# Kernel optimization log

Measured on AMD Instinct MI355X. Metric: run time of the kernel, lower is better.

Reference implementation:

```python
import jax, jax.numpy as jnp
import numpy as np
from jax import lax

DN = ('NCHW', 'OIHW', 'NCHW')


def conv3x3(x, w, b):
    y = lax.conv_general_dilated(x, w, (1, 1), [(1, 1), (1, 1)], dimension_numbers=DN)
    return y + b[None, :, None, None]


def lrelu(x, s):
    return jnp.where(x >= 0, x, s * x)


def layernorm_c(x, g, b, eps=1e-5):
    # LayerNorm over embed_dim; tokens are (h,w), so normalize the channel axis
    m = jnp.mean(x, axis=1, keepdims=True)
    v = jnp.var(x, axis=1, keepdims=True)
    return (x - m) / jnp.sqrt(v + eps) * g[None, :, None, None] + b[None, :, None, None]


def bilateral_corr(x1, x2, md):
    # bilateral cost volume on L2-normalized features:
    # out[b,d,h,w] = <x1n[b,:,h-dy,w-dx], x2n[b,:,h+dy,w+dx]>, (dy,dx) in [-md,md]^2
    def l2n(x):
        return x / jnp.maximum(jnp.linalg.norm(x, axis=1, keepdims=True), 1e-12)
    x1n, x2n = l2n(x1), l2n(x2)
    B, C, H, W = x1.shape
    p1 = jnp.pad(x1n, ((0, 0), (0, 0), (md, md), (md, md)))
    p2 = jnp.pad(x2n, ((0, 0), (0, 0), (md, md), (md, md)))
    outs = []
    for dy in range(-md, md + 1):
        for dx in range(-md, md + 1):
            a = p1[:, :, md - dy:md - dy + H, md - dx:md - dx + W]
            b = p2[:, :, md + dy:md + dy + H, md + dx:md + dx + W]
            outs.append(jnp.sum(a * b, axis=1))
    return jnp.stack(outs, axis=1)  # [B, (2md+1)^2, H, W]


def tail(xt, bi, gln, bln, w0, b0, wr1, br1, wr2, br2, w2, b2, w3, b3, wdec, bdec, wf, bf):
    xt = layernorm_c(xt, gln, bln)
    y = conv3x3(jnp.concatenate([xt, bi], axis=1), w0, b0)
    # resblock(64,64): lrelu(conv2(lrelu(conv1(y))) + y), slope 0.1
    s = y
    r = lrelu(conv3x3(y, wr1, br1), 0.1)
    r = conv3x3(r, wr2, br2) + s
    y = lrelu(r, 0.1)
    y = lrelu(conv3x3(y, w2, b2), 0.2)
    y = lrelu(conv3x3(y, w3, b3), 0.2)
    # ConvTranspose2d(64,64,3,stride=2,pad=1,out_pad=1): lhs-dilated conv with flipped kernel
    wd = jnp.transpose(jnp.flip(wdec, (-2, -1)), (1, 0, 2, 3))  # torch [in,out,kh,kw] -> OIHW
    y = lax.conv_general_dilated(y, wd, (1, 1), [(1, 2), (1, 2)], lhs_dilation=(2, 2), dimension_numbers=DN) + bdec[None, :, None, None]
    flow = conv3x3(y, wf, bf)  # [B, 2, 2H, 2W]
    B, _, H2, W2 = flow.shape
    # F.interpolate(scale_factor=4, mode='bilinear', align_corners=False) * 4
    return jax.image.resize(flow, (B, 2, 4 * H2, 4 * W2), method='bilinear') * 4.0


def setup_inputs():
    key = jax.random.key(0)
    ks = jax.random.split(key, 16)
    B, C, H, W = 4, 256, 96, 160
    md = 3
    r = lambda k, s, sc=0.05: jax.random.normal(k, s, jnp.float32) * sc
    return {
        'x1': jax.random.normal(ks[0], (B, C, H, W), jnp.float32),
        'x2': jax.random.normal(ks[1], (B, C, H, W), jnp.float32),
        'xt': jax.random.normal(ks[2], (B, C, H, W), jnp.float32),
        'gln': jnp.ones((C,), jnp.float32),
        'bln': jnp.zeros((C,), jnp.float32),
        'w0': r(ks[3], (64, C + (2 * md + 1) ** 2, 3, 3)),
        'b0': jnp.zeros((64,), jnp.float32),
        'wr1': r(ks[4], (64, 64, 3, 3)), 'br1': jnp.zeros((64,), jnp.float32),
        'wr2': r(ks[5], (64, 64, 3, 3)), 'br2': jnp.zeros((64,), jnp.float32),
        'w2': r(ks[6], (64, 64, 3, 3)), 'b2': jnp.zeros((64,), jnp.float32),
        'w3': r(ks[7], (64, 64, 3, 3)), 'b3': jnp.zeros((64,), jnp.float32),
        'wdec': r(ks[8], (64, 64, 3, 3)), 'bdec': jnp.zeros((64,), jnp.float32),
        'wf': r(ks[9], (2, 64, 3, 3)), 'bf': jnp.zeros((2,), jnp.float32),
        'corr_range': 3,
    }


def reference(x1, x2, xt, gln, bln, w0, b0, wr1, br1, wr2, br2, w2, b2, w3, b3, wdec, bdec, wf, bf, corr_range):
    bi = bilateral_corr(x1, x2, int(corr_range))
    return tail(xt, bi, gln, bln, w0, b0, wr1, br1, wr2, br2, w2, b2, w3, b3, wdec, bdec, wf, bf)
```

## Files before the change

### kernel.cpp

```cpp
#include <hip/hip_runtime.h>
#include <math.h>

#define HH_ 96
#define WW_ 160
#define HW 15360
#define NPIX 61440
#define CC 256
#define C0 320
#define FF 64
#define H2 192
#define W2 320
#define OHW 61440
#define HO 768
#define WO 1280

typedef __attribute__((ext_vector_type(8))) short short8;
typedef __attribute__((ext_vector_type(4))) float f32x4;

__device__ __forceinline__ float bf2f(ushort u) {
    union { unsigned int i; float f; } v; v.i = ((unsigned int)u) << 16; return v.f;
}
__device__ __forceinline__ ushort f2bf(float f) {
    union { float f; unsigned int i; } v; v.f = f;
    unsigned int u = v.i;
    return (ushort)((u + 0x7FFFu + ((u >> 16) & 1u)) >> 16);
}

__global__ __launch_bounds__(256) void normpack_kernel(
    const float* __restrict__ x1, const float* __restrict__ x2, const float* __restrict__ xt,
    const float* __restrict__ gam, const float* __restrict__ bet,
    ushort* __restrict__ x1c, ushort* __restrict__ x2c,
    ushort* __restrict__ Xhi, float* __restrict__ inv1, float* __restrict__ inv2) {
    __shared__ ushort tile[64 * 258];
    __shared__ float sred[4][64][2];
    const int t = threadIdx.x;
    const int w = t >> 6, l = t & 63;
    const int px4 = l & 15, c_off = l >> 4;
    const int pxt = blockIdx.x, which = blockIdx.y, b = blockIdx.z;
    const float* src = (which == 0 ? x1 : which == 1 ? x2 : xt);
    src += (size_t)b * CC * HW + pxt * 64;

    float s1[4] = {0.f, 0.f, 0.f, 0.f}, s2[4] = {0.f, 0.f, 0.f, 0.f};
#pragma unroll
    for (int it = 0; it < 16; ++it) {
        int c = it * 16 + w * 4 + c_off;
        f32x4 v4 = *(const f32x4*)(src + (size_t)c * HW + px4 * 4);
#pragma unroll
        for (int j = 0; j < 4; ++j) {
            float f = v4[j];
            s1[j] += f; s2[j] += f * f;
            tile[(px4 * 4 + j) * 258 + c] = f2bf(f);
        }
    }
#pragma unroll
    for (int j = 0; j < 4; ++j) {
        s1[j] += __shfl_xor(s1[j], 16); s1[j] += __shfl_xor(s1[j], 32);
        s2[j] += __shfl_xor(s2[j], 16); s2[j] += __shfl_xor(s2[j], 32);
    }
    if (c_off == 0) {
#pragma unroll
        for (int j = 0; j < 4; ++j) {
            sred[w][px4 * 4 + j][0] = s1[j];
            sred[w][px4 * 4 + j][1] = s2[j];
        }
    }
    __syncthreads();

    const int px = t >> 2, grp = t & 3;
    float S1 = sred[0][px][0] + sred[1][px][0] + sred[2][px][0] + sred[3][px][0];
    float S2 = sred[0][px][1] + sred[1][px][1] + sred[2][px][1] + sred[3][px][1];
    const int p = b * HW + pxt * 64 + px;
    const ushort* row = &tile[px * 258];
    if (which < 2) {
        float inv = 1.f / fmaxf(sqrtf(S2), 1e-12f);
        if (grp == 0) (which == 0 ? inv1 : inv2)[p] = inv;
        ushort* dst = (which == 0 ? x1c : x2c) + (size_t)p * CC + grp * 64;
#pragma unroll
        for (int k = 0; k < 8; ++k) {
            short8 o;
#pragma unroll
            for (int h = 0; h < 4; ++h) {
                unsigned int u2 = *(const unsigned int*)(row + grp * 64 + k * 8 + h * 2);
                o[h * 2]     = (short)(u2 & 0xFFFF);
                o[h * 2 + 1] = (short)(u2 >> 16);
            }
            *(short8*)(dst + k * 8) = o;
        }
    } else {
        float m = S1 * (1.f / 256.f);
        float var = fmaxf(S2 * (1.f / 256.f) - m * m, 0.f);
        float rs = rsqrtf(var + 1e-5f);
        ushort* dst = Xhi + (size_t)p * C0 + grp * 64;
#pragma unroll
        for (int k = 0; k < 8; ++k) {
            short8 o;
#pragma unroll
            for (int h = 0; h < 4; ++h) {
                unsigned int u2 = *(const unsigned int*)(row + grp * 64 + k * 8 + h * 2);
                int c = grp * 64 + k * 8 + h * 2;
                float f0 = (bf2f((ushort)(u2 & 0xFFFF)) - m) * rs * gam[c] + bet[c];
                float f1 = (bf2f((ushort)(u2 >> 16)) - m) * rs * gam[c + 1] + bet[c + 1];
                o[h * 2]     = (short)f2bf(f0);
                o[h * 2 + 1] = (short)f2bf(f1);
            }
            *(short8*)(dst + k * 8) = o;
        }
        short8 z = {0, 0, 0, 0, 0, 0, 0, 0};
        *(short8*)(Xhi + (size_t)p * C0 + 256 + grp * 16) = z;
        *(short8*)(Xhi + (size_t)p * C0 + 256 + grp * 16 + 8) = z;
    }
}

__global__ __launch_bounds__(256) void corr_mfma_kernel(
    const ushort* __restrict__ x1c, const ushort* __restrict__ x2c,
    const float* __restrict__ inv1, const float* __restrict__ inv2,
    ushort* __restrict__ Xhi) {
    const int lane = threadIdx.x & 63;
    const int wv = threadIdx.x >> 6;
    const int sid = ((blockIdx.x & 7) * 120) + (blockIdx.x >> 3);
    const int b  = sid / 240;
    const int rem = sid % 240;
    const int uq = rem / 10, xt = rem % 10;
    const int u = uq * 4 + wv;
    const int x0 = xt * 16;
    const int jl = lane & 15;
    const int kg = lane >> 4;
    const short8 zero8 = {0, 0, 0, 0, 0, 0, 0, 0};

    short8 qf[8];
    {
        size_t qb = ((size_t)b * HW + u * WW_ + x0 + jl) * CC + kg * 8;
#pragma unroll
        for (int ks = 0; ks < 8; ++ks)
            qf[ks] = *(const short8*)(x1c + qb + ks * 32);
    }
    float iv1v[4];
#pragma unroll
    for (int r = 0; r < 4; ++r)
        iv1v[r] = inv1[b * HW + u * WW_ + x0 + kg * 4 + r];

    for (int dy = -3; dy <= 3; ++dy) {
        const int y = u + dy;
        if ((unsigned)y >= (unsigned)HH_) continue;
        const int w = u + 2 * dy;
        const bool rowok = (unsigned)w < (unsigned)HH_;

        f32x4 acc0 = (f32x4){0.f, 0.f, 0.f, 0.f};
        f32x4 acc1 = (f32x4){0.f, 0.f, 0.f, 0.f};
        if (rowok) {
#pragma unroll
            for (int nt = 0; nt < 2; ++nt) {
                int kx = x0 - 6 + jl + 16 * nt;
                bool ok = (unsigned)kx < (unsigned)WW_;
                int kxc = min(max(kx, 0), WW_ - 1);
                size_t kb = ((size_t)b * HW + w * WW_ + kxc) * CC + kg * 8;
#pragma unroll
                for (int ks = 0; ks < 8; ++ks) {
                    short8 bv = *(const short8*)(x2c + kb + ks * 32);
                    if (!ok) bv = zero8;
                    if (nt == 0)
                        acc0 = __builtin_amdgcn_mfma_f32_16x16x32_bf16(qf[ks], bv, acc0, 0, 0, 0);
                    else
                        acc1 = __builtin_amdgcn_mfma_f32_16x16x32_bf16(qf[ks], bv, acc1, 0, 0, 0);
                }
            }
        }
#pragma unroll
        for (int nt = 0; nt < 2; ++nt) {
            int j = jl + 16 * nt;
#pragma unroll
            for (int r = 0; r < 4; ++r) {
                int q = kg * 4 + r;
                int tt = j - q - 6;
                if (tt & 1) continue;
                int dx = tt >> 1;
                if (dx < -3 || dx > 3) continue;
                int cx = x0 + q + dx;
                if ((unsigned)cx >= (unsigned)WW_) continue;
                float v = 0.f;
                if (rowok) {
                    int pbx = min(max(x0 + q + 2 * dx, 0), WW_ - 1);
                    float iv2 = inv2[b * HW + w * WW_ + pbx];
                    v = (nt == 0 ? acc0[r] : acc1[r]) * iv1v[r] * iv2;
                }
                size_t o = ((size_t)(b * HW + y * WW_ + cx)) * C0
                         + 256 + (dy + 3) * 7 + (dx + 3);
                Xhi[o] = f2bf(v);
            }
        }
    }
}

__global__ void pack_w_all(const float* __restrict__ w0, const float* __restrict__ wr1,
                           const float* __restrict__ wr2, const float* __restrict__ w2,
                           const float* __restrict__ w3, const float* __restrict__ wdec,
                           ushort* __restrict__ W0, ushort* __restrict__ WR1,
                           ushort* __restrict__ WR2, ushort* __restrict__ W2o,
                           ushort* __restrict__ W3o, ushort* __restrict__ WD) {
    int job = blockIdx.y;
    const float* w = job == 0 ? w0 : job == 1 ? wr1 : job == 2 ? wr2
                   : job == 3 ? w2 : job == 4 ? w3 : wdec;
    ushort* dst = job == 0 ? W0 : job == 1 ? WR1 : job == 2 ? WR2
                : job == 3 ? W2o : job == 4 ? W3o : WD;
    int CinReal = job == 0 ? 305 : 64;
    int KC = job == 0 ? 10 : 2;
    int isDeconv = (job == 5);
    int gid = blockIdx.x * blockDim.x + threadIdx.x;
    int total = 9 * KC * 4 * 64;
    if (gid >= total) return;
    int lane = gid & 63;
    int nt = (gid >> 6) & 3;
    int kc = (gid >> 8) % KC;
    int slot = (gid >> 8) / KC;
    int co = nt * 16 + (lane & 15);
    int ky = slot / 3, kx = slot % 3;
    for (int j = 0; j < 8; ++j) {
        int ci = kc * 32 + (lane >> 4) * 8 + j;
        float v = 0.f;
        if (ci < CinReal) {
            if (isDeconv) v = w[((size_t)(ci * 64 + co) * 3 + (2 - ky)) * 3 + (2 - kx)];
            else          v = w[((size_t)(co * CinReal + ci) * 3 + ky) * 3 + kx];
        }
        dst[(size_t)gid * 8 + j] = f2bf(v);
    }
}

template<int KC>
__global__ __launch_bounds__(256, 4) void conv_lds_t(
    const ushort* __restrict__ Ahi,
    const ushort* __restrict__ Whi,
    const float* __restrict__ bias,
    ushort* __restrict__ Ohi,
    const ushort* __restrict__ Rhi,
    float slope, int act, int hasres) {
    constexpr int CIN = KC * 32;
    __shared__ ushort lds[2 * 3488];
    const int t = threadIdx.x;
    const int lane = t & 63;
    const int wave = t >> 6;
    const int kg = lane >> 4;
    const int jl = lane & 15;
    const short8 zero8 = {0, 0, 0, 0, 0, 0, 0, 0};

    const int sid = ((blockIdx.x & 7) * 120) + (blockIdx.x >> 3);
    const int b0 = sid / 240;
    const int rm = sid % 240;
    const int yq = rm / 10, xw = rm % 10;
    const int y0 = yq * 4;
    const int x0 = xw * 16;
    const size_t rowbase = (size_t)b0 * HW;

    f32x4 acc[4];
#pragma unroll
    for (int nt = 0; nt < 4; ++nt) acc[nt] = (f32x4){0.f, 0.f, 0.f, 0.f};

    auto stage = [&](ushort* buf, int kc) {
#pragma unroll
        for (int i = 0; i < 2; ++i) {
            int e = t + i * 256;
            if (e < 432) {
                int kge = e & 3;
                int q = e >> 2;
                int pe = q % 18;
                int re = q / 18;
                int gy = y0 - 1 + re, gx = x0 - 1 + pe;
                bool ok = ((unsigned)gy < 96u) && ((unsigned)gx < 160u);
                short8 vh = zero8;
                if (ok) {
                    size_t ga = ((rowbase + gy * WW_ + gx) * (size_t)CIN) + kc * 32 + kge * 8;
                    vh = *(const short8*)(Ahi + ga);
                }
                *(short8*)(buf + kge * 872 + (re * 18 + pe) * 8) = vh;
            }
        }
    };

    stage(lds, 0);

#pragma unroll 1
    for (int kc = 0; kc < KC; ++kc) {
        __syncthreads();
        if (kc + 1 < KC) stage(lds + ((kc + 1) & 1) * 3488, kc + 1);
        const ushort* bufc = lds + (kc & 1) * 3488;
#pragma unroll
        for (int tap = 0; tap < 9; ++tap) {
            const int dy = tap / 3 - 1, dx = tap % 3 - 1;
            const int abase = kg * 872 + (wave + dy + 1) * 144 + (jl + dx + 1) * 8;
            short8 ah = *(const short8*)(bufc + abase);
            const ushort* wt = Whi + (size_t)(tap * KC + kc) * 2048;
#pragma unroll
            for (int nt = 0; nt < 4; ++nt) {
                short8 bh = *(const short8*)(wt + (nt * 64 + lane) * 8);
                acc[nt] = __builtin_amdgcn_mfma_f32_16x16x32_bf16(ah, bh, acc[nt], 0, 0, 0);
            }
        }
    }

#pragma unroll
    for (int r = 0; r < 4; ++r) {
        size_t pr = rowbase + (y0 + wave) * WW_ + x0 + kg * 4 + r;
#pragma unroll
        for (int nt = 0; nt < 4; ++nt) {
            int co = nt * 16 + jl;
            float vv = acc[nt][r] + bias[co];
            size_t oo = pr * 64 + co;
            if (hasres) vv += bf2f(Rhi[oo]);
            if (act) vv = vv >= 0.f ? vv : vv * slope;
            Ohi[oo] = f2bf(vv);
        }
    }
}

__global__ __launch_bounds__(256, 2) void deconv_fused_kernel(
    const ushort* __restrict__ Ahi,
    const ushort* __restrict__ Whi,
    const float* __restrict__ bias,
    ushort* __restrict__ decb) {
    const int lane = threadIdx.x & 63;
    const int wave = threadIdx.x >> 6;
    const int kg = lane >> 4;
    const short8 zero8 = {0, 0, 0, 0, 0, 0, 0, 0};

    const int sid = ((blockIdx.x & 7) * 120) + (blockIdx.x >> 3);
    const int b0 = sid / 240;
    const int rm = sid % 240;
    const int yq = rm / 10, xh = rm % 10;
    const int y0 = yq * 4 + wave;
    const int x0 = xh * 16;
    const size_t rowbase = (size_t)b0 * HW;

    f32x4 acc[4][4];
#pragma unroll
    for (int p = 0; p < 4; ++p)
#pragma unroll
        for (int nt = 0; nt < 4; ++nt) acc[p][nt] = (f32x4){0.f, 0.f, 0.f, 0.f};

    const int nuse[4]   = {4, 2, 2, 1};
    const int upar[4][4] = {{0, 1, 2, 3}, {1, 3, -1, -1}, {2, 3, -1, -1}, {3, -1, -1, -1}};
    const int uslt[4][4] = {{4, 3, 1, 0}, {5, 2, -1, -1}, {7, 6, -1, -1}, {8, -1, -1, -1}};

#pragma unroll
    for (int o = 0; o < 4; ++o) {
        const int ody = o >> 1, odx = o & 1;
        int yy = y0 + ody, xx = x0 + (lane & 15) + odx;
        bool v = (unsigned)yy < 96u && (unsigned)xx < 160u;
        int yyc = min(yy, 95), xxc = min(xx, 159);
        size_t a = (rowbase + yyc * WW_ + xxc) * 64 + kg * 8;
#pragma unroll
        for (int kc = 0; kc < 2; ++kc) {
            short8 ah = *(const short8*)(Ahi + a + kc * 32);
            if (!v) ah = zero8;
#pragma unroll
            for (int u = 0; u < 4; ++u) {
                if (u >= nuse[o]) break;
                int par = upar[o][u], slot = uslt[o][u];
#pragma unroll
                for (int nt = 0; nt < 4; ++nt) {
                    short8 bh = *(const short8*)(Whi + ((size_t)slot * 2 + kc) * 2048
                                                 + ((size_t)nt * 64 + lane) * 8);
                    acc[par][nt] = __builtin_amdgcn_mfma_f32_16x16x32_bf16(ah, bh, acc[par][nt], 0, 0, 0);
                }
            }
        }
    }

#pragma unroll
    for (int r = 0; r < 4; ++r) {
        int x2 = x0 + kg * 4 + r;
#pragma unroll
        for (int par = 0; par < 4; ++par) {
            int py = par >> 1, px = par & 1;
            size_t po = ((size_t)b0 * H2 + 2 * y0 + py) * W2 + 2 * x2 + px;
#pragma unroll
            for (int nt = 0; nt < 4; ++nt) {
                int co = nt * 16 + (lane & 15);
                decb[po * 64 + co] = f2bf(acc[par][nt][r] + bias[co]);
            }
        }
    }
}

__global__ __launch_bounds__(256) void flow_kernel(const ushort* __restrict__ decb,
                                                   const float* __restrict__ wf,
                                                   const float* __restrict__ bf2v,
                                                   float* __restrict__ flow) {
    __shared__ float wsm[1152];
    for (int i = threadIdx.x; i < 1152; i += 256) wsm[i] = wf[i];
    __syncthreads();
    int fid = ((blockIdx.x & 7) * 120) + (blockIdx.x >> 3);
    int p = fid * 256 + threadIdx.x;
    if (p >= 4 * OHW) return;
    int b = p / OHW, rem = p % OHW, oy = rem / W2, ox = rem % W2;
    float a0 = bf2v[0], a1 = bf2v[1];
    for (int ky = 0; ky < 3; ++ky) {
        int yy = oy + ky - 1;
        if ((unsigned)yy >= (unsigned)H2) continue;
        for (int kx = 0; kx < 3; ++kx) {
            int xx = ox + kx - 1;
            if ((unsigned)xx >= (unsigned)W2) continue;
            size_t base = ((size_t)b * OHW + yy * W2 + xx) * 64;
            int tap = ky * 3 + kx;
#pragma unroll
            for (int c8 = 0; c8 < 8; ++c8) {
                short8 v8 = *(const short8*)(decb + base + c8 * 8);
#pragma unroll
                for (int j = 0; j < 8; ++j) {
                    float f = bf2f((ushort)v8[j]);
                    int ci = c8 * 8 + j;
                    a0 += f * wsm[ci * 9 + tap];
                    a1 += f * wsm[(64 + ci) * 9 + tap];
                }
            }
        }
    }
    flow[(size_t)(b * 2 + 0) * OHW + rem] = a0;
    flow[(size_t)(b * 2 + 1) * OHW + rem] = a1;
}

__global__ __launch_bounds__(256) void resize_kernel(const float* __restrict__ flow,
                                                     float* __restrict__ out) {
    int idx = blockIdx.x * blockDim.x + threadIdx.x;
    int total = 4 * 2 * HO * (WO / 4);
    if (idx >= total) return;
    int qx = idx % (WO / 4);
    int oy = (idx / (WO / 4)) % HO;
    int c  = (idx / ((WO / 4) * HO)) % 2;
    int b  = idx / ((WO / 4) * HO * 2);

    float sy = (oy + 0.5f) * 0.25f - 0.5f;
    int y0 = (int)floorf(sy);
    float fy = sy - y0;
    int y0c = min(max(y0, 0), H2 - 1);
    int y1c = min(max(y0 + 1, 0), H2 - 1);
    const float* r0 = flow + ((size_t)(b * 2 + c) * H2 + y0c) * W2;
    const float* r1 = flow + ((size_t)(b * 2 + c) * H2 + y1c) * W2;
    int xm = max(qx - 1, 0), xp = min(qx + 1, W2 - 1);
    float fm = (1.f - fy) * r0[xm] + fy * r1[xm];
    float f0 = (1.f - fy) * r0[qx] + fy * r1[qx];
    float fp = (1.f - fy) * r0[xp] + fy * r1[xp];
    f32x4 o;
    o[0] = (0.375f * fm + 0.625f * f0) * 4.0f;
    o[1] = (0.125f * fm + 0.875f * f0) * 4.0f;
    o[2] = (0.875f * f0 + 0.125f * fp) * 4.0f;
    o[3] = (0.625f * f0 + 0.375f * fp) * 4.0f;
    *(f32x4*)(out + (((size_t)(b * 2 + c) * HO + oy) * WO) + qx * 4) = o;
}

extern "C" void kernel_launch(void* const* d_in, const int* in_sizes, int n_in,
                              void* d_out, int out_size, void* d_ws, size_t ws_size,
                              hipStream_t stream) {
    const float* x1   = (const float*)d_in[0];
    const float* x2   = (const float*)d_in[1];
    const float* xt   = (const float*)d_in[2];
    const float* gln  = (const float*)d_in[3];
    const float* bln  = (const float*)d_in[4];
    const float* w0   = (const float*)d_in[5];
    const float* b0   = (const float*)d_in[6];
    const float* wr1  = (const float*)d_in[7];
    const float* br1  = (const float*)d_in[8];
    const float* wr2  = (const float*)d_in[9];
    const float* br2  = (const float*)d_in[10];
    const float* w2   = (const float*)d_in[11];
    const float* b2   = (const float*)d_in[12];
    const float* w3   = (const float*)d_in[13];
    const float* b3   = (const float*)d_in[14];
    const float* wdec = (const float*)d_in[15];
    const float* bdec = (const float*)d_in[16];
    const float* wf   = (const float*)d_in[17];
    const float* bfv  = (const float*)d_in[18];
    float* out = (float*)d_out;

    char* ws = (char*)d_ws;
    ushort* x1c  = (ushort*)(ws + 0);
    ushort* x2c  = (ushort*)(ws + 31457280);
    ushort* X0hi = (ushort*)(ws + 62914560);
    ushort* y0hi = (ushort*)(ws + 102236160);
    ushort* t1hi = (ushort*)(ws + 110100480);
    ushort* t2hi = (ushort*)(ws + 117964800);
    ushort* decb = (ushort*)(ws + 0);
    float*  flowb = (float*)(ws + 62914560);
    char* wp = ws + 125829120;
    ushort* W0hi  = (ushort*)(wp);
    ushort* WR1hi = (ushort*)(wp + 368640);
    ushort* WR2hi = (ushort*)(wp + 442368);
    ushort* W2hi  = (ushort*)(wp + 516096);
    ushort* W3hi  = (ushort*)(wp + 589824);
    ushort* WDhi  = (ushort*)(wp + 663552);
    float*  inv1  = (float*)(wp + 786432);
    float*  inv2  = (float*)(wp + 1048576);

    pack_w_all<<<dim3(90, 6), 256, 0, stream>>>(w0, wr1, wr2, w2, w3, wdec,
        W0hi, WR1hi, WR2hi, W2hi, W3hi, WDhi);

    normpack_kernel<<<dim3(240, 3, 4), 256, 0, stream>>>(
        x1, x2, xt, gln, bln, x1c, x2c, X0hi, inv1, inv2);
    corr_mfma_kernel<<<960, 256, 0, stream>>>(x1c, x2c, inv1, inv2, X0hi);

    conv_lds_t<10><<<960, 256, 0, stream>>>(X0hi, W0hi, b0, y0hi, nullptr, 0.f, 0, 0);
    conv_lds_t<2><<<960, 256, 0, stream>>>(y0hi, WR1hi, br1, t1hi, nullptr, 0.1f, 1, 0);
    conv_lds_t<2><<<960, 256, 0, stream>>>(t1hi, WR2hi, br2, t2hi, y0hi, 0.1f, 1, 1);
    conv_lds_t<2><<<960, 256, 0, stream>>>(t2hi, W2hi, b2, t1hi, nullptr, 0.2f, 1, 0);
    conv_lds_t<2><<<960, 256, 0, stream>>>(t1hi, W3hi, b3, t2hi, nullptr, 0.2f, 1, 0);
    deconv_fused_kernel<<<960, 256, 0, stream>>>(t2hi, WDhi, bdec, decb);

    flow_kernel<<<960, 256, 0, stream>>>(decb, wf, bfv, flowb);
    resize_kernel<<<7680, 256, 0, stream>>>(flowb, out);

    (void)in_sizes; (void)n_in; (void)out_size; (void)ws_size;
}
```

Measured before the change: 357.7 us.

## Split work across more blocks in normpack, 64-ch convs, deconv and flow

Halves the per-block tile in normpack (32 pixels) and gives the 64-channel convs a new kernel where each block covers 2 rows and each wave computes only half of the output channels, with the LDS halo double-buffered over the two K chunks. The deconv also splits output channels across wave pairs, and the flow kernel splits the 64 input channels across two threads that combine their sums with a shuffle. Grids double to 1920 blocks and launch bounds are raised to allow more resident blocks per CU. The aim is better occupancy and latency hiding on small grids, at the cost of more redundant halo loads, and each wave now reuses its loaded activations across fewer MFMAs.

```diff
diff --git a/kernel.cpp b/kernel.cpp
--- a/kernel.cpp
+++ b/kernel.cpp
@@ -31,19 +31,20 @@
     const float* __restrict__ gam, const float* __restrict__ bet,
     ushort* __restrict__ x1c, ushort* __restrict__ x2c,
     ushort* __restrict__ Xhi, float* __restrict__ inv1, float* __restrict__ inv2) {
-    __shared__ ushort tile[64 * 258];
-    __shared__ float sred[4][64][2];
+    __shared__ ushort tile[32 * 258];
+    __shared__ float sred[4][32][2];
     const int t = threadIdx.x;
     const int w = t >> 6, l = t & 63;
-    const int px4 = l & 15, c_off = l >> 4;
+    const int px4 = l & 7;
+    const int cbase = t >> 3;
     const int pxt = blockIdx.x, which = blockIdx.y, b = blockIdx.z;
     const float* src = (which == 0 ? x1 : which == 1 ? x2 : xt);
-    src += (size_t)b * CC * HW + pxt * 64;
+    src += (size_t)b * CC * HW + pxt * 32;
 
     float s1[4] = {0.f, 0.f, 0.f, 0.f}, s2[4] = {0.f, 0.f, 0.f, 0.f};
 #pragma unroll
-    for (int it = 0; it < 16; ++it) {
-        int c = it * 16 + w * 4 + c_off;
+    for (int it = 0; it < 8; ++it) {
+        int c = it * 32 + cbase;
         f32x4 v4 = *(const f32x4*)(src + (size_t)c * HW + px4 * 4);
 #pragma unroll
         for (int j = 0; j < 4; ++j) {
@@ -54,10 +55,10 @@
     }
 #pragma unroll
     for (int j = 0; j < 4; ++j) {
-        s1[j] += __shfl_xor(s1[j], 16); s1[j] += __shfl_xor(s1[j], 32);
-        s2[j] += __shfl_xor(s2[j], 16); s2[j] += __shfl_xor(s2[j], 32);
-    }
-    if (c_off == 0) {
+        s1[j] += __shfl_xor(s1[j], 8);  s1[j] += __shfl_xor(s1[j], 16); s1[j] += __shfl_xor(s1[j], 32);
+        s2[j] += __shfl_xor(s2[j], 8);  s2[j] += __shfl_xor(s2[j], 16); s2[j] += __shfl_xor(s2[j], 32);
+    }
+    if ((l >> 3) == 0) {
 #pragma unroll
         for (int j = 0; j < 4; ++j) {
             sred[w][px4 * 4 + j][0] = s1[j];
@@ -66,21 +67,21 @@
     }
     __syncthreads();
 
-    const int px = t >> 2, grp = t & 3;
+    const int px = t >> 3, grp = t & 7;
     float S1 = sred[0][px][0] + sred[1][px][0] + sred[2][px][0] + sred[3][px][0];
     float S2 = sred[0][px][1] + sred[1][px][1] + sred[2][px][1] + sred[3][px][1];
-    const int p = b * HW + pxt * 64 + px;
+    const int p = b * HW + pxt * 32 + px;
     const ushort* row = &tile[px * 258];
     if (which < 2) {
         float inv = 1.f / fmaxf(sqrtf(S2), 1e-12f);
         if (grp == 0) (which == 0 ? inv1 : inv2)[p] = inv;
-        ushort* dst = (which == 0 ? x1c : x2c) + (size_t)p * CC + grp * 64;
-#pragma unroll
-        for (int k = 0; k < 8; ++k) {
+        ushort* dst = (which == 0 ? x1c : x2c) + (size_t)p * CC + grp * 32;
+#pragma unroll
+        for (int k = 0; k < 4; ++k) {
             short8 o;
 #pragma unroll
             for (int h = 0; h < 4; ++h) {
-                unsigned int u2 = *(const unsigned int*)(row + grp * 64 + k * 8 + h * 2);
+                unsigned int u2 = *(const unsigned int*)(row + grp * 32 + k * 8 + h * 2);
                 o[h * 2]     = (short)(u2 & 0xFFFF);
                 o[h * 2 + 1] = (short)(u2 >> 16);
             }
@@ -90,14 +91,14 @@
         float m = S1 * (1.f / 256.f);
         float var = fmaxf(S2 * (1.f / 256.f) - m * m, 0.f);
         float rs = rsqrtf(var + 1e-5f);
-        ushort* dst = Xhi + (size_t)p * C0 + grp * 64;
-#pragma unroll
-        for (int k = 0; k < 8; ++k) {
+        ushort* dst = Xhi + (size_t)p * C0 + grp * 32;
+#pragma unroll
+        for (int k = 0; k < 4; ++k) {
             short8 o;
 #pragma unroll
             for (int h = 0; h < 4; ++h) {
-                unsigned int u2 = *(const unsigned int*)(row + grp * 64 + k * 8 + h * 2);
-                int c = grp * 64 + k * 8 + h * 2;
+                unsigned int u2 = *(const unsigned int*)(row + grp * 32 + k * 8 + h * 2);
+                int c = grp * 32 + k * 8 + h * 2;
                 float f0 = (bf2f((ushort)(u2 & 0xFFFF)) - m) * rs * gam[c] + bet[c];
                 float f1 = (bf2f((ushort)(u2 >> 16)) - m) * rs * gam[c + 1] + bet[c + 1];
                 o[h * 2]     = (short)f2bf(f0);
@@ -105,9 +106,11 @@
             }
             *(short8*)(dst + k * 8) = o;
         }
-        short8 z = {0, 0, 0, 0, 0, 0, 0, 0};
-        *(short8*)(Xhi + (size_t)p * C0 + 256 + grp * 16) = z;
-        *(short8*)(Xhi + (size_t)p * C0 + 256 + grp * 16 + 8) = z;
+        if (grp < 4) {
+            short8 z = {0, 0, 0, 0, 0, 0, 0, 0};
+            *(short8*)(Xhi + (size_t)p * C0 + 256 + grp * 16) = z;
+            *(short8*)(Xhi + (size_t)p * C0 + 256 + grp * 16 + 8) = z;
+        }
     }
 }
 
@@ -311,29 +314,118 @@
     }
 }
 
-__global__ __launch_bounds__(256, 2) void deconv_fused_kernel(
+__global__ __launch_bounds__(256, 8) void conv_lds2(
+    const ushort* __restrict__ Ahi,
+    const ushort* __restrict__ Whi,
+    const float* __restrict__ bias,
+    ushort* __restrict__ Ohi,
+    const ushort* __restrict__ Rhi,
+    float slope, int act, int hasres) {
+    __shared__ ushort lds[2 * 2336];
+    const int t = threadIdx.x;
+    const int lane = t & 63;
+    const int wave = t >> 6;
+    const int row_w = wave >> 1;
+    const int coh = wave & 1;
+    const int kg = lane >> 4;
+    const int jl = lane & 15;
+    const short8 zero8 = {0, 0, 0, 0, 0, 0, 0, 0};
+
+    const int sid = ((blockIdx.x & 7) * 240) + (blockIdx.x >> 3);
+    const int b0 = sid / 480;
+    const int rm = sid % 480;
+    const int yp = rm / 10, xw = rm % 10;
+    const int y0 = yp * 2;
+    const int x0 = xw * 16;
+    const size_t rowbase = (size_t)b0 * HW;
+
+    f32x4 acc[2];
+    acc[0] = (f32x4){0.f, 0.f, 0.f, 0.f};
+    acc[1] = (f32x4){0.f, 0.f, 0.f, 0.f};
+
+    auto stage = [&](ushort* buf, int kc) {
+#pragma unroll
+        for (int i = 0; i < 2; ++i) {
+            int e = t + i * 256;
+            if (e < 288) {
+                int kge = e & 3;
+                int q = e >> 2;
+                int pe = q % 18;
+                int re = q / 18;
+                int gy = y0 - 1 + re, gx = x0 - 1 + pe;
+                bool ok = ((unsigned)gy < 96u) && ((unsigned)gx < 160u);
+                short8 vh = zero8;
+                if (ok) {
+                    size_t ga = ((rowbase + gy * WW_ + gx) * 64) + kc * 32 + kge * 8;
+                    vh = *(const short8*)(Ahi + ga);
+                }
+                *(short8*)(buf + kge * 584 + (re * 18 + pe) * 8) = vh;
+            }
+        }
+    };
+
+    stage(lds, 0);
+
+#pragma unroll 1
+    for (int kc = 0; kc < 2; ++kc) {
+        __syncthreads();
+        if (kc == 0) stage(lds + 2336, 1);
+        const ushort* bufc = lds + (kc & 1) * 2336;
+#pragma unroll
+        for (int tap = 0; tap < 9; ++tap) {
+            const int dy = tap / 3 - 1, dx = tap % 3 - 1;
+            const int abase = kg * 584 + (row_w + dy + 1) * 144 + (jl + dx + 1) * 8;
+            short8 ah = *(const short8*)(bufc + abase);
+            const ushort* wt = Whi + (size_t)(tap * 2 + kc) * 2048;
+#pragma unroll
+            for (int nt = 0; nt < 2; ++nt) {
+                short8 bh = *(const short8*)(wt + (((coh << 1) | nt) * 64 + lane) * 8);
+                acc[nt] = __builtin_amdgcn_mfma_f32_16x16x32_bf16(ah, bh, acc[nt], 0, 0, 0);
+            }
+        }
+    }
+
+#pragma unroll
+    for (int r = 0; r < 4; ++r) {
+        size_t pr = rowbase + (y0 + row_w) * WW_ + x0 + kg * 4 + r;
+#pragma unroll
+        for (int nt = 0; nt < 2; ++nt) {
+            int co = ((coh << 1) | nt) * 16 + jl;
+            float vv = acc[nt][r] + bias[co];
+            size_t oo = pr * 64 + co;
+            if (hasres) vv += bf2f(Rhi[oo]);
+            if (act) vv = vv >= 0.f ? vv : vv * slope;
+            Ohi[oo] = f2bf(vv);
+        }
+    }
+}
+
+__global__ __launch_bounds__(256, 6) void deconv_fused_kernel(
     const ushort* __restrict__ Ahi,
     const ushort* __restrict__ Whi,
     const float* __restrict__ bias,
     ushort* __restrict__ decb) {
     const int lane = threadIdx.x & 63;
     const int wave = threadIdx.x >> 6;
+    const int row_w = wave >> 1;
+    const int coh = wave & 1;
     const int kg = lane >> 4;
     const short8 zero8 = {0, 0, 0, 0, 0, 0, 0, 0};
 
-    const int sid = ((blockIdx.x & 7) * 120) + (blockIdx.x >> 3);
-    const int b0 = sid / 240;
-    const int rm = sid % 240;
-    const int yq = rm / 10, xh = rm % 10;
-    const int y0 = yq * 4 + wave;
+    const int sid = ((blockIdx.x & 7) * 240) + (blockIdx.x >> 3);
+    const int b0 = sid / 480;
+    const int rm = sid % 480;
+    const int yp = rm / 10, xh = rm % 10;
+    const int y0 = yp * 2 + row_w;
     const int x0 = xh * 16;
     const size_t rowbase = (size_t)b0 * HW;
 
-    f32x4 acc[4][4];
-#pragma unroll
-    for (int p = 0; p < 4; ++p)
-#pragma unroll
-        for (int nt = 0; nt < 4; ++nt) acc[p][nt] = (f32x4){0.f, 0.f, 0.f, 0.f};
+    f32x4 acc[4][2];
+#pragma unroll
+    for (int p = 0; p < 4; ++p) {
+        acc[p][0] = (f32x4){0.f, 0.f, 0.f, 0.f};
+        acc[p][1] = (f32x4){0.f, 0.f, 0.f, 0.f};
+    }
 
     const int nuse[4]   = {4, 2, 2, 1};
     const int upar[4][4] = {{0, 1, 2, 3}, {1, 3, -1, -1}, {2, 3, -1, -1}, {3, -1, -1, -1}};
@@ -355,9 +447,9 @@
                 if (u >= nuse[o]) break;
                 int par = upar[o][u], slot = uslt[o][u];
 #pragma unroll
-                for (int nt = 0; nt < 4; ++nt) {
+                for (int nt = 0; nt < 2; ++nt) {
                     short8 bh = *(const short8*)(Whi + ((size_t)slot * 2 + kc) * 2048
-                                                 + ((size_t)nt * 64 + lane) * 8);
+                                                 + (((coh << 1) | nt) * 64 + lane) * 8);
                     acc[par][nt] = __builtin_amdgcn_mfma_f32_16x16x32_bf16(ah, bh, acc[par][nt], 0, 0, 0);
                 }
             }
@@ -372,8 +464,8 @@
             int py = par >> 1, px = par & 1;
             size_t po = ((size_t)b0 * H2 + 2 * y0 + py) * W2 + 2 * x2 + px;
 #pragma unroll
-            for (int nt = 0; nt < 4; ++nt) {
-                int co = nt * 16 + (lane & 15);
+            for (int nt = 0; nt < 2; ++nt) {
+                int co = ((coh << 1) | nt) * 16 + (lane & 15);
                 decb[po * 64 + co] = f2bf(acc[par][nt][r] + bias[co]);
             }
         }
@@ -387,11 +479,12 @@
     __shared__ float wsm[1152];
     for (int i = threadIdx.x; i < 1152; i += 256) wsm[i] = wf[i];
     __syncthreads();
-    int fid = ((blockIdx.x & 7) * 120) + (blockIdx.x >> 3);
-    int p = fid * 256 + threadIdx.x;
+    int fid = ((blockIdx.x & 7) * 240) + (blockIdx.x >> 3);
+    int tid = fid * 256 + threadIdx.x;
+    int p = tid >> 1, half = tid & 1;
     if (p >= 4 * OHW) return;
     int b = p / OHW, rem = p % OHW, oy = rem / W2, ox = rem % W2;
-    float a0 = bf2v[0], a1 = bf2v[1];
+    float a0 = 0.f, a1 = 0.f;
     for (int ky = 0; ky < 3; ++ky) {
         int yy = oy + ky - 1;
         if ((unsigned)yy >= (unsigned)H2) continue;
@@ -401,20 +494,25 @@
             size_t base = ((size_t)b * OHW + yy * W2 + xx) * 64;
             int tap = ky * 3 + kx;
 #pragma unroll
-            for (int c8 = 0; c8 < 8; ++c8) {
-                short8 v8 = *(const short8*)(decb + base + c8 * 8);
+            for (int c8 = 0; c8 < 4; ++c8) {
+                int cg = half * 4 + c8;
+                short8 v8 = *(const short8*)(decb + base + cg * 8);
 #pragma unroll
                 for (int j = 0; j < 8; ++j) {
                     float f = bf2f((ushort)v8[j]);
-                    int ci = c8 * 8 + j;
+                    int ci = cg * 8 + j;
                     a0 += f * wsm[ci * 9 + tap];
                     a1 += f * wsm[(64 + ci) * 9 + tap];
                 }
             }
         }
     }
-    flow[(size_t)(b * 2 + 0) * OHW + rem] = a0;
-    flow[(size_t)(b * 2 + 1) * OHW + rem] = a1;
+    a0 += __shfl_xor(a0, 1);
+    a1 += __shfl_xor(a1, 1);
+    if (half == 0) {
+        flow[(size_t)(b * 2 + 0) * OHW + rem] = a0 + bf2v[0];
+        flow[(size_t)(b * 2 + 1) * OHW + rem] = a1 + bf2v[1];
+    }
 }
 
 __global__ __launch_bounds__(256) void resize_kernel(const float* __restrict__ flow,
@@ -492,18 +590,18 @@
     pack_w_all<<<dim3(90, 6), 256, 0, stream>>>(w0, wr1, wr2, w2, w3, wdec,
         W0hi, WR1hi, WR2hi, W2hi, W3hi, WDhi);
 
-    normpack_kernel<<<dim3(240, 3, 4), 256, 0, stream>>>(
+    normpack_kernel<<<dim3(480, 3, 4), 256, 0, stream>>>(
         x1, x2, xt, gln, bln, x1c, x2c, X0hi, inv1, inv2);
     corr_mfma_kernel<<<960, 256, 0, stream>>>(x1c, x2c, inv1, inv2, X0hi);
 
     conv_lds_t<10><<<960, 256, 0, stream>>>(X0hi, W0hi, b0, y0hi, nullptr, 0.f, 0, 0);
-    conv_lds_t<2><<<960, 256, 0, stream>>>(y0hi, WR1hi, br1, t1hi, nullptr, 0.1f, 1, 0);
-    conv_lds_t<2><<<960, 256, 0, stream>>>(t1hi, WR2hi, br2, t2hi, y0hi, 0.1f, 1, 1);
-    conv_lds_t<2><<<960, 256, 0, stream>>>(t2hi, W2hi, b2, t1hi, nullptr, 0.2f, 1, 0);
-    conv_lds_t<2><<<960, 256, 0, stream>>>(t1hi, W3hi, b3, t2hi, nullptr, 0.2f, 1, 0);
-    deconv_fused_kernel<<<960, 256, 0, stream>>>(t2hi, WDhi, bdec, decb);
-
-    flow_kernel<<<960, 256, 0, stream>>>(decb, wf, bfv, flowb);
+    conv_lds2<<<1920, 256, 0, stream>>>(y0hi, WR1hi, br1, t1hi, nullptr, 0.1f, 1, 0);
+    conv_lds2<<<1920, 256, 0, stream>>>(t1hi, WR2hi, br2, t2hi, y0hi, 0.1f, 1, 1);
+    conv_lds2<<<1920, 256, 0, stream>>>(t2hi, W2hi, b2, t1hi, nullptr, 0.2f, 1, 0);
+    conv_lds2<<<1920, 256, 0, stream>>>(t1hi, W3hi, b3, t2hi, nullptr, 0.2f, 1, 0);
+    deconv_fused_kernel<<<1920, 256, 0, stream>>>(t2hi, WDhi, bdec, decb);
+
+    flow_kernel<<<1920, 256, 0, stream>>>(decb, wf, bfv, flowb);
     resize_kernel<<<7680, 256, 0, stream>>>(flowb, out);
 
     (void)in_sizes; (void)n_in; (void)out_size; (void)ws_size;
```

Measured after the change: 336.6 us. 5.9% less time.
